# Optimization experiments

Hardware: AMD Instinct MI355X
Metric: run time of the kernel (lower is better)

The kernel has to match this reference:

```python
import jax, jax.numpy as jnp
import numpy as np

D_IN = 1024
D_OUT = 1024
NUM_HEADS = 16
HEAD_DIM = D_OUT // NUM_HEADS


def setup_inputs() -> dict:
    key = jax.random.key(0)
    k1, k2, k3, k4 = jax.random.split(key, 4)
    x = jax.random.normal(k1, (2, 2048, D_IN), dtype=jnp.float32)
    # qkv Linear (bias=False): weight [3*d_out, d_in]
    w_qkv = jax.random.normal(k2, (3 * D_OUT, D_IN), dtype=jnp.float32) * (1.0 / np.sqrt(D_IN))
    # proj Linear (default bias=True): weight [d_out, d_out], bias [d_out]
    w_proj = jax.random.normal(k3, (D_OUT, D_OUT), dtype=jnp.float32) * (1.0 / np.sqrt(D_OUT))
    b_proj = jax.random.normal(k4, (D_OUT,), dtype=jnp.float32) * 0.01
    return {"x": x, "w_qkv": w_qkv, "w_proj": w_proj, "b_proj": b_proj}


def reference(x, w_qkv, w_proj, b_proj):
    B, S, E = x.shape
    qkv = jnp.einsum("bse,fe->bsf", x, w_qkv)                 # [B,S,3*d_out]
    qkv = qkv.reshape(B, S, 3, NUM_HEADS, HEAD_DIM)
    qkv = jnp.transpose(qkv, (2, 0, 3, 1, 4))                  # [3,B,H,S,D]
    q, k, v = qkv[0], qkv[1], qkv[2]
    scores = jnp.einsum("bhqd,bhkd->bhqk", q, k)               # [B,H,S,S]
    causal = jnp.triu(jnp.ones((S, S), dtype=bool), k=1)
    scores = jnp.where(causal, -jnp.inf, scores)
    # NOTE: source divides by head_dim**(-0.5), i.e. multiplies by sqrt(head_dim)
    scores = scores / (HEAD_DIM ** -0.5)
    attn = jax.nn.softmax(scores, axis=-1)
    ctx = jnp.einsum("bhqk,bhkd->bhqd", attn, v)               # [B,H,S,D]
    ctx = jnp.transpose(ctx, (0, 2, 1, 3)).reshape(B, S, E)
    return jnp.einsum("bse,fe->bsf", ctx, w_proj) + b_proj
```

## Files before the change

### kernel.cpp

```cpp
#include <hip/hip_runtime.h>

typedef _Float16 f16;
typedef _Float16 f16x4 __attribute__((ext_vector_type(4)));
typedef _Float16 f16x8 __attribute__((ext_vector_type(8)));
typedef float f32x4 __attribute__((ext_vector_type(4)));

#define MFMA16(a, b, c) __builtin_amdgcn_mfma_f32_16x16x32_f16(a, b, c, 0, 0, 0)
#define QSCALE 11.5415603f

typedef const __attribute__((address_space(1))) void* gp1_t;
typedef __attribute__((address_space(3))) void* lp3_t;
__device__ __forceinline__ void gld16(const void* g, void* l) {
    __builtin_amdgcn_global_load_lds((gp1_t)g, (lp3_t)l, 16, 0, 0);
}

__global__ __launch_bounds__(256) void cvt_all(
    const float* __restrict__ x, const float* __restrict__ wq, const float* __restrict__ wp,
    f16* __restrict__ xh, f16* __restrict__ wqh, f16* __restrict__ wph)
{
    int i = blockIdx.x * 256 + threadIdx.x;
    const float4* src; f16x4* dst; int off;
    if (i < 1048576)      { src = (const float4*)x;  dst = (f16x4*)xh;  off = i; }
    else if (i < 1835008) { src = (const float4*)wq; dst = (f16x4*)wqh; off = i - 1048576; }
    else                  { src = (const float4*)wp; dst = (f16x4*)wph; off = i - 1835008; }
    float4 v = src[off];
    f16x4 o = { (f16)v.x, (f16)v.y, (f16)v.z, (f16)v.w };
    dst[off] = o;
}

template<int EPI>
__global__ __launch_bounds__(256) void gemm_k(
    const f16* __restrict__ A, const f16* __restrict__ B, int K,
    f16* __restrict__ qb, f16* __restrict__ kb, f16* __restrict__ vt,
    float* __restrict__ outF, const float* __restrict__ bias)
{
    __shared__ f16 as[128 * 32];
    __shared__ f16 bs[128 * 32];
    const int t = threadIdx.x;
    const int m0 = blockIdx.y * 128, n0 = blockIdx.x * 128;
    const int lane = t & 63, wv = t >> 6;
    const int wm = wv >> 1, wn = wv & 1;
    const int lr = lane & 15, g = lane >> 4;
    const int srow = lane >> 2, schk = (lane & 3) * 8;
    const f16* Ab = A + (size_t)m0 * K;
    const f16* Bb = B + (size_t)n0 * K;
    f32x4 acc[4][4] = {};

    for (int k0 = 0; k0 < K; k0 += 32) {
        __syncthreads();
        #pragma unroll
        for (int i2 = 0; i2 < 2; ++i2) {
            const int r0 = wv * 32 + i2 * 16;
            gld16(&Ab[(size_t)(r0 + srow) * K + k0 + schk], &as[r0 * 32]);
            gld16(&Bb[(size_t)(r0 + srow) * K + k0 + schk], &bs[r0 * 32]);
        }
        __syncthreads();
        f16x8 af[4], bf[4];
        #pragma unroll
        for (int mt = 0; mt < 4; ++mt)
            af[mt] = *reinterpret_cast<const f16x8*>(&as[(wm * 64 + mt * 16 + lr) * 32 + g * 8]);
        #pragma unroll
        for (int nt = 0; nt < 4; ++nt)
            bf[nt] = *reinterpret_cast<const f16x8*>(&bs[(wn * 64 + nt * 16 + lr) * 32 + g * 8]);
        #pragma unroll
        for (int mt = 0; mt < 4; ++mt)
            #pragma unroll
            for (int nt = 0; nt < 4; ++nt)
                acc[mt][nt] = MFMA16(af[mt], bf[nt], acc[mt][nt]);
    }

    #pragma unroll
    for (int mt = 0; mt < 4; ++mt) {
        #pragma unroll
        for (int nt = 0; nt < 4; ++nt) {
            const int n = n0 + wn * 64 + nt * 16 + lr;
            const int s0 = m0 + wm * 64 + mt * 16 + 4 * g;
            if (EPI == 0) {
                const int which = n >> 10, h = (n >> 6) & 15, d = n & 63;
                const int b = s0 >> 11, s = s0 & 2047;
                if (which == 2) {
                    f16x4 vv;
                    #pragma unroll
                    for (int i = 0; i < 4; ++i) vv[i] = (f16)acc[mt][nt][i];
                    *reinterpret_cast<f16x4*>(&vt[((size_t)((b << 4) + h) * 64 + d) * 2048 + s]) = vv;
                } else {
                    f16* dst = which ? kb : qb;
                    const float sc = which ? 1.0f : QSCALE;
                    #pragma unroll
                    for (int i = 0; i < 4; ++i)
                        dst[((size_t)((b << 4) + h) * 2048 + (s + i)) * 64 + d] = (f16)(acc[mt][nt][i] * sc);
                }
            } else {
                #pragma unroll
                for (int i = 0; i < 4; ++i)
                    outF[(size_t)(s0 + i) * 1024 + n] = acc[mt][nt][i] + bias[n];
            }
        }
    }
}

__global__ __launch_bounds__(64) void attn_k(
    const f16* __restrict__ Q, const f16* __restrict__ K, const f16* __restrict__ VT,
    f16* __restrict__ ctx)
{
    __shared__ f16 lp[32][72];
    const int lane = threadIdx.x;
    const int lr = lane & 15, g = lane >> 4;
    const int bid = blockIdx.x;
    const int j = 63 - (bid >> 5);
    const int bh = bid & 31;
    const int b = bh >> 4, h = bh & 15;
    const size_t base = (size_t)bh * (2048 * 64);
    const f16* Qb = Q + base;
    const f16* Kb = K + base;
    const f16* Vb = VT + base;
    const int q0 = j << 5;

    f16x8 qf[2][2];
    #pragma unroll
    for (int nt = 0; nt < 2; ++nt)
        #pragma unroll
        for (int ks = 0; ks < 2; ++ks)
            qf[nt][ks] = *reinterpret_cast<const f16x8*>(&Qb[(size_t)(q0 + nt * 16 + lr) * 64 + ks * 32 + g * 8]);

    f32x4 o[4][2] = {};
    float mrun[2] = { -1e30f, -1e30f };
    float lrun[2] = { 0.f, 0.f };
    const int ntiles = (j >> 1) + 1;

#define ATTN_TILE(KV0, MTMAX, MASKED) do {                                              \
    const int kv0_ = (KV0);                                                             \
    f32x4 st[MTMAX][2] = {};                                                            \
    _Pragma("unroll")                                                                   \
    for (int mt = 0; mt < MTMAX; ++mt) {                                                \
        f16x8 ak[2];                                                                    \
        _Pragma("unroll")                                                               \
        for (int ks = 0; ks < 2; ++ks)                                                  \
            ak[ks] = *reinterpret_cast<const f16x8*>(                                   \
                &Kb[(size_t)(kv0_ + mt * 16 + lr) * 64 + ks * 32 + g * 8]);             \
        _Pragma("unroll")                                                               \
        for (int nt = 0; nt < 2; ++nt)                                                  \
            _Pragma("unroll")                                                           \
            for (int ks = 0; ks < 2; ++ks)                                              \
                st[mt][nt] = MFMA16(ak[ks], qf[nt][ks], st[mt][nt]);                    \
    }                                                                                   \
    _Pragma("unroll")                                                                   \
    for (int nt = 0; nt < 2; ++nt) {                                                    \
        const int qrow_ = q0 + nt * 16 + lr;                                            \
        float mloc = -1e30f;                                                            \
        _Pragma("unroll")                                                               \
        for (int mt = 0; mt < MTMAX; ++mt)                                              \
            _Pragma("unroll")                                                           \
            for (int i = 0; i < 4; ++i) {                                               \
                float sv = st[mt][nt][i];                                               \
                if (MASKED) {                                                           \
                    int kkk = kv0_ + mt * 16 + 4 * g + i;                               \
                    sv = (kkk <= qrow_) ? sv : -1e30f;                                  \
                    st[mt][nt][i] = sv;                                                 \
                }                                                                       \
                mloc = fmaxf(mloc, sv);                                                 \
            }                                                                           \
        mloc = fmaxf(mloc, __shfl_xor(mloc, 16));                                       \
        mloc = fmaxf(mloc, __shfl_xor(mloc, 32));                                       \
        if (__any(mloc > mrun[nt] + 8.0f)) {          \
            float mnew = fmaxf(mrun[nt], mloc);                                         \
            float sc = exp2f(mrun[nt] - mnew);                                          \
            lrun[nt] *= sc;                                                             \
            _Pragma("unroll")                                                           \
            for (int mo = 0; mo < 4; ++mo)                                              \
                _Pragma("unroll")                                                       \
                for (int i = 0; i < 4; ++i) o[mo][nt][i] *= sc;                         \
            mrun[nt] = mnew;                                                            \
        }                                                                               \
        float ls = 0.f;                                                                 \
        _Pragma("unroll")                                                               \
        for (int mt = 0; mt < MTMAX; ++mt) {                                            \
            f16x4 pk;                                                                   \
            _Pragma("unroll")                                                           \
            for (int i = 0; i < 4; ++i) {                                               \
                float p = exp2f(st[mt][nt][i] - mrun[nt]);                              \
                ls += p; pk[i] = (f16)p;                                                \
            }                                                                           \
            *reinterpret_cast<f16x4*>(&lp[nt * 16 + lr][mt * 16 + 4 * g]) = pk;         \
        }                                                                               \
        ls += __shfl_xor(ls, 16);                                                       \
        ls += __shfl_xor(ls, 32);                                                       \
        lrun[nt] += ls;                                                                 \
    }                                                                                   \
    {                                                                                   \
        constexpr int PVKS = (MTMAX) / 2;                                               \
        f16x8 pf[2][PVKS];                                                              \
        _Pragma("unroll")                                                               \
        for (int nt = 0; nt < 2; ++nt)                                                  \
            _Pragma("unroll")                                                           \
            for (int ks = 0; ks < PVKS; ++ks)                                           \
                pf[nt][ks] = *reinterpret_cast<const f16x8*>(                           \
                    &lp[nt * 16 + lr][ks * 32 + g * 8]);                                \
        _Pragma("unroll")                                                               \
        for (int mo = 0; mo < 4; ++mo) {                                                \
            f16x8 av[PVKS];                                                             \
            _Pragma("unroll")                                                           \
            for (int ks = 0; ks < PVKS; ++ks)                                           \
                av[ks] = *reinterpret_cast<const f16x8*>(                               \
                    &Vb[(size_t)(mo * 16 + lr) * 2048 + kv0_ + ks * 32 + g * 8]);       \
            _Pragma("unroll")                                                           \
            for (int nt = 0; nt < 2; ++nt)                                              \
                _Pragma("unroll")                                                       \
                for (int ks = 0; ks < PVKS; ++ks)                                       \
                    o[mo][nt] = MFMA16(av[ks], pf[nt][ks], o[mo][nt]);                  \
        }                                                                               \
    }                                                                                   \
} while (0)

    for (int tt = 0; tt < ntiles - 1; ++tt)
        ATTN_TILE(tt << 6, 4, false);
    {
        const int kvl = (ntiles - 1) << 6;
        if (j & 1) ATTN_TILE(kvl, 4, true);
        else       ATTN_TILE(kvl, 2, true);
    }
#undef ATTN_TILE

    #pragma unroll
    for (int nt = 0; nt < 2; ++nt) {
        const float inv = 1.0f / lrun[nt];
        const int qrow = q0 + nt * 16 + lr;
        const size_t rowoff = ((size_t)(b * 2048 + qrow)) * 1024 + h * 64;
        #pragma unroll
        for (int mo = 0; mo < 4; ++mo) {
            f16x4 ov;
            #pragma unroll
            for (int i = 0; i < 4; ++i) ov[i] = (f16)(o[mo][nt][i] * inv);
            *reinterpret_cast<f16x4*>(&ctx[rowoff + mo * 16 + 4 * g]) = ov;
        }
    }
}

extern "C" void kernel_launch(void* const* d_in, const int* in_sizes, int n_in,
                              void* d_out, int out_size, void* d_ws, size_t ws_size,
                              hipStream_t stream) {
    const float* x      = (const float*)d_in[0];
    const float* w_qkv  = (const float*)d_in[1];
    const float* w_proj = (const float*)d_in[2];
    const float* b_proj = (const float*)d_in[3];
    float* out = (float*)d_out;

    char* p = (char*)d_ws;
    f16* xh     = (f16*)p; p += (size_t)4096 * 1024 * 2;
    f16* wqkvh  = (f16*)p; p += (size_t)3072 * 1024 * 2;
    f16* wprojh = (f16*)p; p += (size_t)1024 * 1024 * 2;
    f16* qbuf   = (f16*)p; p += (size_t)2 * 16 * 2048 * 64 * 2;
    f16* kbuf   = (f16*)p; p += (size_t)2 * 16 * 2048 * 64 * 2;
    f16* vtbuf  = (f16*)p; p += (size_t)2 * 16 * 64 * 2048 * 2;
    f16* ctx    = (f16*)p; p += (size_t)4096 * 1024 * 2;

    cvt_all<<<8192, 256, 0, stream>>>(x, w_qkv, w_proj, xh, wqkvh, wprojh);

    gemm_k<0><<<dim3(24, 32), 256, 0, stream>>>(xh, wqkvh, 1024, qbuf, kbuf, vtbuf, nullptr, nullptr);

    attn_k<<<2048, 64, 0, stream>>>(qbuf, kbuf, vtbuf, ctx);

    gemm_k<1><<<dim3(8, 32), 256, 0, stream>>>(ctx, wprojh, 1024, nullptr, nullptr, nullptr, out, b_proj);
}
```

Measured before the change: 224.2 us.

## Split long causal query blocks across two workgroups and merge with combine kernel

```diff
diff --git a/kernel.cpp b/kernel.cpp
--- a/kernel.cpp
+++ b/kernel.cpp
@@ -101,13 +101,16 @@
 
 __global__ __launch_bounds__(64) void attn_k(
     const f16* __restrict__ Q, const f16* __restrict__ K, const f16* __restrict__ VT,
-    f16* __restrict__ ctx)
+    f16* __restrict__ ctx, f16* __restrict__ opart,
+    float* __restrict__ mpart, float* __restrict__ lpart)
 {
     __shared__ f16 lp[32][72];
     const int lane = threadIdx.x;
     const int lr = lane & 15, g = lane >> 4;
     const int bid = blockIdx.x;
-    const int j = 63 - (bid >> 5);
+    int j, s; bool split;
+    if (bid < 2048) { split = true;  j = 63 - (bid >> 6); s = (bid >> 5) & 1; }
+    else            { split = false; j = 31 - ((bid - 2048) >> 5); s = 0; }
     const int bh = bid & 31;
     const int b = bh >> 4, h = bh & 15;
     const size_t base = (size_t)bh * (2048 * 64);
@@ -115,6 +118,11 @@
     const f16* Kb = K + base;
     const f16* Vb = VT + base;
     const int q0 = j << 5;
+    const int ntt = (j >> 1) + 1;
+    const int H = (ntt + 1) >> 1;
+    const int t0 = split ? (s ? H : 0) : 0;
+    const int t1 = split ? (s ? ntt : H) : ntt;
+    const bool diag = (t1 == ntt);
 
     f16x8 qf[2][2];
     #pragma unroll
@@ -125,8 +133,7 @@
 
     f32x4 o[4][2] = {};
     float mrun[2] = { -1e30f, -1e30f };
-    float lrun[2] = { 0.f, 0.f };
-    const int ntiles = (j >> 1) + 1;
+    float lsum[2] = { 0.f, 0.f };
 
 #define ATTN_TILE(KV0, MTMAX, MASKED) do {                                              \
     const int kv0_ = (KV0);                                                             \
@@ -162,10 +169,10 @@
             }                                                                           \
         mloc = fmaxf(mloc, __shfl_xor(mloc, 16));                                       \
         mloc = fmaxf(mloc, __shfl_xor(mloc, 32));                                       \
-        if (__any(mloc > mrun[nt] + 8.0f)) {          \
+        if (__any(mloc > mrun[nt] + 8.0f)) {                             \
             float mnew = fmaxf(mrun[nt], mloc);                                         \
             float sc = exp2f(mrun[nt] - mnew);                                          \
-            lrun[nt] *= sc;                                                             \
+            lsum[nt] *= sc;                                                             \
             _Pragma("unroll")                                                           \
             for (int mo = 0; mo < 4; ++mo)                                              \
                 _Pragma("unroll")                                                       \
@@ -183,9 +190,7 @@
             }                                                                           \
             *reinterpret_cast<f16x4*>(&lp[nt * 16 + lr][mt * 16 + 4 * g]) = pk;         \
         }                                                                               \
-        ls += __shfl_xor(ls, 16);                                                       \
-        ls += __shfl_xor(ls, 32);                                                       \
-        lrun[nt] += ls;                                                                 \
+        lsum[nt] += ls;                                                                 \
     }                                                                                   \
     {                                                                                   \
         constexpr int PVKS = (MTMAX) / 2;                                               \
@@ -212,10 +217,11 @@
     }                                                                                   \
 } while (0)
 
-    for (int tt = 0; tt < ntiles - 1; ++tt)
+    const int tEnd = t1 - (diag ? 1 : 0);
+    for (int tt = t0; tt < tEnd; ++tt)
         ATTN_TILE(tt << 6, 4, false);
-    {
-        const int kvl = (ntiles - 1) << 6;
+    if (diag) {
+        const int kvl = (ntt - 1) << 6;
         if (j & 1) ATTN_TILE(kvl, 4, true);
         else       ATTN_TILE(kvl, 2, true);
     }
@@ -223,17 +229,59 @@
 
     #pragma unroll
     for (int nt = 0; nt < 2; ++nt) {
-        const float inv = 1.0f / lrun[nt];
-        const int qrow = q0 + nt * 16 + lr;
-        const size_t rowoff = ((size_t)(b * 2048 + qrow)) * 1024 + h * 64;
-        #pragma unroll
-        for (int mo = 0; mo < 4; ++mo) {
-            f16x4 ov;
+        float l = lsum[nt];
+        l += __shfl_xor(l, 16);
+        l += __shfl_xor(l, 32);
+        const float inv = 1.0f / l;
+        const int ql = nt * 16 + lr;
+        if (!split) {
+            const size_t rowoff = ((size_t)(b * 2048 + q0 + ql)) * 1024 + h * 64;
             #pragma unroll
-            for (int i = 0; i < 4; ++i) ov[i] = (f16)(o[mo][nt][i] * inv);
-            *reinterpret_cast<f16x4*>(&ctx[rowoff + mo * 16 + 4 * g]) = ov;
+            for (int mo = 0; mo < 4; ++mo) {
+                f16x4 ov;
+                #pragma unroll
+                for (int i = 0; i < 4; ++i) ov[i] = (f16)(o[mo][nt][i] * inv);
+                *reinterpret_cast<f16x4*>(&ctx[rowoff + mo * 16 + 4 * g]) = ov;
+            }
+        } else {
+            const int mi = ((s * 32 + bh) * 32 + (j - 32)) * 32 + ql;
+            #pragma unroll
+            for (int mo = 0; mo < 4; ++mo) {
+                f16x4 ov;
+                #pragma unroll
+                for (int i = 0; i < 4; ++i) ov[i] = (f16)(o[mo][nt][i] * inv);
+                *reinterpret_cast<f16x4*>(&opart[(size_t)mi * 64 + mo * 16 + 4 * g]) = ov;
+            }
+            if (g == 0) { mpart[mi] = mrun[nt]; lpart[mi] = l; }
         }
     }
+}
+
+__global__ __launch_bounds__(256) void combine_k(
+    const f16* __restrict__ opart, const float* __restrict__ mpart,
+    const float* __restrict__ lpart, f16* __restrict__ ctx)
+{
+    const int blk = blockIdx.x;
+    const int bh = blk >> 5, jj = blk & 31;
+    const int b = bh >> 4, h = bh & 15;
+    const int t = threadIdx.x;
+    const int q = t >> 3, dc = (t & 7) * 8;
+    const int mi0 = (bh * 32 + jj) * 32 + q;
+    const int mi1 = mi0 + 32768;
+    const float m0 = mpart[mi0], m1 = mpart[mi1];
+    const float l0 = lpart[mi0], l1 = lpart[mi1];
+    const float mx = fmaxf(m0, m1);
+    const float a0 = l0 * exp2f(m0 - mx);
+    const float a1 = l1 * exp2f(m1 - mx);
+    const float r = 1.0f / (a0 + a1);
+    const float c0 = a0 * r, c1 = a1 * r;
+    f16x8 v0 = *reinterpret_cast<const f16x8*>(&opart[(size_t)mi0 * 64 + dc]);
+    f16x8 v1 = *reinterpret_cast<const f16x8*>(&opart[(size_t)mi1 * 64 + dc]);
+    f16x8 outv;
+    #pragma unroll
+    for (int i = 0; i < 8; ++i) outv[i] = (f16)(c0 * (float)v0[i] + c1 * (float)v1[i]);
+    const int qg = (jj + 32) * 32 + q;
+    *reinterpret_cast<f16x8*>(&ctx[((size_t)(b * 2048 + qg)) * 1024 + h * 64 + dc]) = outv;
 }
 
 extern "C" void kernel_launch(void* const* d_in, const int* in_sizes, int n_in,
@@ -254,11 +302,17 @@
     f16* vtbuf  = (f16*)p; p += (size_t)2 * 16 * 64 * 2048 * 2;
     f16* ctx    = (f16*)p; p += (size_t)4096 * 1024 * 2;
 
+    f16*   opart = xh;
+    float* mpart = (float*)wqkvh;
+    float* lpart = mpart + 65536;
+
     cvt_all<<<8192, 256, 0, stream>>>(x, w_qkv, w_proj, xh, wqkvh, wprojh);
 
     gemm_k<0><<<dim3(24, 32), 256, 0, stream>>>(xh, wqkvh, 1024, qbuf, kbuf, vtbuf, nullptr, nullptr);
 
-    attn_k<<<2048, 64, 0, stream>>>(qbuf, kbuf, vtbuf, ctx);
+    attn_k<<<3072, 64, 0, stream>>>(qbuf, kbuf, vtbuf, ctx, opart, mpart, lpart);
+
+    combine_k<<<1024, 256, 0, stream>>>(opart, mpart, lpart, ctx);
 
     gemm_k<1><<<dim3(8, 32), 256, 0, stream>>>(ctx, wprojh, 1024, nullptr, nullptr, nullptr, out, b_proj);
 }
```

Result: no change. 223.5 us (-0.3%).
